# Optimization experiments

Measured on AMD Instinct MI355X. Metric: run time of the kernel, lower is better.

Reference implementation:

```python
import math
import jax, jax.numpy as jnp
import numpy as np

D_MODEL = 768
EXPAND = 2
D_INNER = EXPAND * D_MODEL  # 1536
D_STATE = 16
D_CONV = 4
DT_RANK = math.ceil(D_INNER / 16)  # 96
B, L = 2, 2048
LN_EPS = 1e-5


def setup_inputs() -> dict:
    key = jax.random.key(0)
    ks = jax.random.split(key, 10)
    x = jax.random.normal(ks[0], (B, L, D_MODEL), dtype=jnp.float32)
    ln_g = jnp.ones((D_MODEL,), jnp.float32)
    ln_b = jnp.zeros((D_MODEL,), jnp.float32)
    W_in = jax.random.normal(ks[1], (D_MODEL, 2 * D_INNER), jnp.float32) / np.sqrt(D_MODEL)
    conv_w = jax.random.normal(ks[2], (D_INNER, 1, D_CONV), jnp.float32) / np.sqrt(D_CONV)
    conv_b = jax.random.normal(ks[3], (D_INNER,), jnp.float32) * 0.02
    W_xproj = jax.random.normal(ks[4], (D_INNER, DT_RANK + 2 * D_STATE), jnp.float32) / np.sqrt(D_INNER)
    W_dt = jax.random.normal(ks[5], (DT_RANK, D_INNER), jnp.float32) / np.sqrt(DT_RANK)
    # dt bias init: inverse-softplus of dt ~ LogUniform(1e-3, 1e-1)
    dt = jnp.exp(jax.random.uniform(ks[6], (D_INNER,)) * (math.log(0.1) - math.log(0.001)) + math.log(0.001))
    b_dt = dt + jnp.log(-jnp.expm1(-dt))
    log_A = jnp.log(jnp.tile(jnp.arange(1, D_STATE + 1, dtype=jnp.float32), (D_INNER, 1)))  # (d_inner, N)
    D_param = jnp.ones((D_INNER,), jnp.float32)
    W_out = jax.random.normal(ks[7], (D_INNER, D_MODEL), jnp.float32) / np.sqrt(D_INNER)
    return dict(x=x, ln_g=ln_g, ln_b=ln_b, W_in=W_in, conv_w=conv_w, conv_b=conv_b,
                W_xproj=W_xproj, W_dt=W_dt, b_dt=b_dt, log_A=log_A, D_param=D_param, W_out=W_out)


def _mamba_block(x, ln_g, ln_b, W_in, conv_w, conv_b, W_xproj, W_dt, b_dt, log_A, D_param, W_out):
    residual = x
    # LayerNorm
    mu = jnp.mean(x, axis=-1, keepdims=True)
    var = jnp.var(x, axis=-1, keepdims=True)
    xn = (x - mu) * jax.lax.rsqrt(var + LN_EPS) * ln_g + ln_b
    # in projection -> (u, v)
    uv = xn @ W_in  # (B, L, 2*d_inner)
    u, v = jnp.split(uv, 2, axis=-1)
    # causal depthwise conv1d along length (torch pads both sides then truncates -> left pad only)
    u_c = jnp.transpose(u, (0, 2, 1))  # (B, d_inner, L)
    u_c = jax.lax.conv_general_dilated(
        u_c, conv_w, window_strides=(1,), padding=[(D_CONV - 1, 0)],
        dimension_numbers=('NCH', 'OIH', 'NCH'), feature_group_count=D_INNER)
    u_c = u_c + conv_b[None, :, None]
    u = jnp.transpose(u_c, (0, 2, 1))  # (B, L, d_inner)
    u = jax.nn.silu(u)
    # Selective SSM
    x_dbl = u @ W_xproj  # (B, L, dt_rank + 2N)
    dlt, Bm, Cm = jnp.split(x_dbl, [DT_RANK, DT_RANK + D_STATE], axis=-1)
    delta = jax.nn.softplus(dlt @ W_dt + b_dt)  # (B, L, d_inner)
    A = -jnp.exp(log_A)  # (d_inner, N)
    A_bar = jnp.exp(jnp.einsum('bld,dn->bldn', delta, A))         # discretized A
    Bu = jnp.einsum('bld,bln,bld->bldn', delta, Bm, u)            # B_bar * u
    # parallel scan: h_k = A_bar_k * h_{k-1} + Bu_k
    def comb(e1, e2):
        a1, b1 = e1
        a2, b2 = e2
        return a1 * a2, a2 * b1 + b2
    _, h = jax.lax.associative_scan(comb, (A_bar, Bu), axis=1)
    y = jnp.einsum('bldn,bln->bld', h, Cm) + u * D_param
    # gate + residual
    y = y * jax.nn.silu(v)
    return y @ W_out + residual


def reference(x, ln_g, ln_b, W_in, conv_w, conv_b, W_xproj, W_dt, b_dt, log_A, D_param, W_out):
    return _mamba_block(x, ln_g, ln_b, W_in, conv_w, conv_b, W_xproj, W_dt, b_dt, log_A, D_param, W_out)
```

## Files before the change

### kernel.cpp

```cpp
#include <hip/hip_runtime.h>

#define D_MODEL 768
#define D_INNER 1536
#define D_STATE 16
#define DT_RANK 96
#define BB 2
#define LL 2048
#define TT (BB*LL)
#define NC 64
#define CL 32
#define SKK 4
#define LOG2E 1.44269504f

typedef unsigned short u16;
typedef short bf16x8 __attribute__((ext_vector_type(8)));
typedef unsigned short u16x8 __attribute__((ext_vector_type(8)));
typedef float f32x4  __attribute__((ext_vector_type(4)));

__device__ __forceinline__ float bf2f(u16 u) {
    union { unsigned int i; float f; } c; c.i = ((unsigned int)u) << 16; return c.f;
}
__device__ __forceinline__ u16 f2bf(float f) {
    union { float f; unsigned int i; } c; c.f = f;
    unsigned int x = c.i;
    return (u16)((x + 0x7fffu + ((x >> 16) & 1u)) >> 16);
}
__device__ __forceinline__ float bfu_lo(unsigned int u) {
    union { unsigned int i; float f; } c; c.i = u << 16; return c.f;
}
__device__ __forceinline__ float bfu_hi(unsigned int u) {
    union { unsigned int i; float f; } c; c.i = u & 0xFFFF0000u; return c.f;
}
__device__ __forceinline__ float ldx(const void* p, size_t i, bool f32) {
    return f32 ? ((const float*)p)[i] : bf2f(((const u16*)p)[i]);
}

__device__ __forceinline__ void gload16(const u16* g, u16* l) {
    __builtin_amdgcn_global_load_lds(
        (const __attribute__((address_space(1))) unsigned int*)g,
        (__attribute__((address_space(3))) unsigned int*)l, 16, 0, 0);
}

__global__ void detect_kernel(const void* x, int* flag)
{
    __shared__ int bad;
    if (threadIdx.x == 0) bad = 0;
    __syncthreads();
    const u16* p = (const u16*)x;
    int local = 0;
    for (int i = threadIdx.x; i < 2048; i += 256) {
        const float v = bf2f(p[2 * i]);
        if (!(fabsf(v) < 1e4f)) local = 1;
    }
    if (local) atomicOr(&bad, 1);
    __syncthreads();
    if (threadIdx.x == 0) *flag = bad;
}

__global__ __launch_bounds__(256) void transpose_all_kernel(
    const void* __restrict__ W_in, const void* __restrict__ W_xp,
    const void* __restrict__ W_dt, const void* __restrict__ W_out,
    u16* __restrict__ WtIn, u16* __restrict__ WtXp,
    u16* __restrict__ WtDt, u16* __restrict__ WtOut,
    const int* __restrict__ flagp)
{
    const bool f32 = (*flagp != 0);
    int bid = blockIdx.x;
    const void* src; u16* dst; int K, N, bx, by;
    if (bid < 576)      { src = W_in;  dst = WtIn;  K = 768;  N = 3072; bx = bid % 48; by = bid / 48; }
    else if (bid < 624) { bid -= 576; src = W_xp;  dst = WtXp;  K = 1536; N = 128;  bx = bid % 2;  by = bid / 2; }
    else if (bid < 672) { bid -= 624; src = W_dt;  dst = WtDt;  K = 96;   N = 1536; bx = bid % 24; by = bid / 24; }
    else                { bid -= 672; src = W_out; dst = WtOut; K = 1536; N = 768;  bx = bid % 12; by = bid / 12; }
    __shared__ u16 tile[64][72];
    const int t  = threadIdx.x;
    const int n0 = bx * 64, k0 = by * 64;
    {
        const int r = t >> 2, c = (t & 3) * 16;
        const int k = k0 + r;
        if (k < K) {
            #pragma unroll
            for (int i = 0; i < 16; ++i)
                tile[r][c + i] = f2bf(ldx(src, (size_t)k * N + n0 + c + i, f32));
        }
    }
    __syncthreads();
    {
        const int nl = t >> 2, kl = (t & 3) * 16;
        const int n = n0 + nl;
        #pragma unroll
        for (int i = 0; i < 16; ++i) {
            const int k = k0 + kl + i;
            if (k < K) dst[(size_t)n * K + k] = tile[kl + i][nl];
        }
    }
}

__global__ __launch_bounds__(256) void ln_kernel(const void* __restrict__ x,
    const void* __restrict__ g, const void* __restrict__ b, u16* __restrict__ xn,
    const int* __restrict__ flagp)
{
    const bool f32 = (*flagp != 0);
    const int tok = blockIdx.x;
    const int tid = threadIdx.x;
    const size_t base = (size_t)tok * D_MODEL;
    float v[3];
    v[0] = ldx(x, base + tid, f32);
    v[1] = ldx(x, base + tid + 256, f32);
    v[2] = ldx(x, base + tid + 512, f32);
    float s = v[0] + v[1] + v[2];
    float q = v[0]*v[0] + v[1]*v[1] + v[2]*v[2];
    #pragma unroll
    for (int o = 32; o > 0; o >>= 1) {
        s += __shfl_down(s, o, 64);
        q += __shfl_down(q, o, 64);
    }
    __shared__ float ss[4], qq[4];
    if ((tid & 63) == 0) { ss[tid >> 6] = s; qq[tid >> 6] = q; }
    __syncthreads();
    const float S = ss[0] + ss[1] + ss[2] + ss[3];
    const float Q = qq[0] + qq[1] + qq[2] + qq[3];
    const float mu  = S * (1.f / D_MODEL);
    const float var = Q * (1.f / D_MODEL) - mu * mu;
    const float rs  = rsqrtf(var + 1e-5f);
    u16* outr = xn + base;
    #pragma unroll
    for (int i = 0; i < 3; ++i) {
        const int c = tid + i * 256;
        outr[c] = f2bf((v[i] - mu) * rs * ldx(g, c, f32) + ldx(b, c, f32));
    }
}

template<int EPI>
__global__ __launch_bounds__(256) void mfma_gemm(
    const u16* __restrict__ A, const u16* __restrict__ Bt,
    u16* __restrict__ C, void* __restrict__ Cout, const void* __restrict__ aux,
    float* __restrict__ Cf, const int* __restrict__ flagp,
    int Kslice, int lda, int ldbt, int ldc)
{
    const bool f32 = (*flagp != 0);
    __shared__ alignas(16) u16 As[64 * 32];
    __shared__ alignas(16) u16 Bs[64 * 32];
    const int tid  = threadIdx.x;
    const int wave = tid >> 6, lane = tid & 63;
    const int lrow = lane & 15, quad = lane >> 4;
    const int row0 = blockIdx.y * 64, col0 = blockIdx.x * 64;
    const int k0   = blockIdx.z * Kslice;
    const int srow = wave * 16 + (lane >> 2);
    const int skk  = (lane & 3) * 8;
    u16* lA = &As[wave * 512];
    u16* lB = &Bs[wave * 512];
    const u16* gA = A  + (size_t)(row0 + srow) * lda  + skk;
    const u16* gB = Bt + (size_t)(col0 + srow) * ldbt + skk;
    f32x4 acc[4] = {{0.f,0.f,0.f,0.f},{0.f,0.f,0.f,0.f},{0.f,0.f,0.f,0.f},{0.f,0.f,0.f,0.f}};
    for (int kt = k0; kt < k0 + Kslice; kt += 32) {
        gload16(gA + kt, lA);
        gload16(gB + kt, lB);
        __syncthreads();
        const bf16x8 af = *(const bf16x8*)(&As[(wave * 16 + lrow) * 32 + quad * 8]);
        #pragma unroll
        for (int t = 0; t < 4; ++t) {
            const bf16x8 bf_ = *(const bf16x8*)(&Bs[(t * 16 + lrow) * 32 + quad * 8]);
            acc[t] = __builtin_amdgcn_mfma_f32_16x16x32_bf16(af, bf_, acc[t], 0, 0, 0);
        }
        __syncthreads();
    }
    #pragma unroll
    for (int t = 0; t < 4; ++t) {
        #pragma unroll
        for (int r = 0; r < 4; ++r) {
            const int row = row0 + wave * 16 + quad * 4 + r;
            const int col = col0 + t * 16 + lrow;
            const size_t idx = (size_t)row * ldc + col;
            float vv = acc[t][r];
            if (EPI == 1) {
                vv += ldx(aux, col, f32);
                vv = (vv > 20.f) ? vv : log1pf(__expf(vv));
                C[idx] = f2bf(vv);
            } else if (EPI == 2) {
                vv += ldx(aux, idx, f32);
                if (f32) ((float*)Cout)[idx] = vv;
                else     ((u16*)Cout)[idx]   = f2bf(vv);
            } else if (EPI == 3) {
                atomicAdd(&Cf[idx], vv);
            } else {
                C[idx] = f2bf(vv);
            }
        }
    }
}

template<int EPI>
__global__ __launch_bounds__(256) void mfma_gemm128(
    const u16* __restrict__ A, const u16* __restrict__ Bt,
    u16* __restrict__ C, void* __restrict__ Cout, const void* __restrict__ aux,
    const int* __restrict__ flagp,
    int K, int lda, int ldbt, int ldc)
{
    const bool f32 = (*flagp != 0);
    __shared__ alignas(16) u16 As[128 * 32];
    __shared__ alignas(16) u16 Bs[128 * 32];
    const int tid  = threadIdx.x;
    const int wave = tid >> 6, lane = tid & 63;
    const int lrow = lane & 15, quad = lane >> 4;
    const int wy = wave >> 1, wx = wave & 1;
    const int row0 = blockIdx.y * 128, col0 = blockIdx.x * 128;
    const int skk = (lane & 3) * 8;
    const int r0 = wave * 16 + (lane >> 2);
    const int r1 = r0 + 64;
    u16* lA0 = &As[wave * 512];
    u16* lA1 = &As[(wave + 4) * 512];
    u16* lB0 = &Bs[wave * 512];
    u16* lB1 = &Bs[(wave + 4) * 512];
    const u16* gA0 = A  + (size_t)(row0 + r0) * lda  + skk;
    const u16* gA1 = A  + (size_t)(row0 + r1) * lda  + skk;
    const u16* gB0 = Bt + (size_t)(col0 + r0) * ldbt + skk;
    const u16* gB1 = Bt + (size_t)(col0 + r1) * ldbt + skk;
    f32x4 acc[4][4];
    #pragma unroll
    for (int i = 0; i < 4; ++i)
        #pragma unroll
        for (int j = 0; j < 4; ++j) acc[i][j] = (f32x4){0.f,0.f,0.f,0.f};
    for (int kt = 0; kt < K; kt += 32) {
        gload16(gA0 + kt, lA0);
        gload16(gA1 + kt, lA1);
        gload16(gB0 + kt, lB0);
        gload16(gB1 + kt, lB1);
        __syncthreads();
        bf16x8 af[4], bf_[4];
        #pragma unroll
        for (int i = 0; i < 4; ++i)
            af[i] = *(const bf16x8*)(&As[(wy * 64 + i * 16 + lrow) * 32 + quad * 8]);
        #pragma unroll
        for (int j = 0; j < 4; ++j)
            bf_[j] = *(const bf16x8*)(&Bs[(wx * 64 + j * 16 + lrow) * 32 + quad * 8]);
        #pragma unroll
        for (int i = 0; i < 4; ++i)
            #pragma unroll
            for (int j = 0; j < 4; ++j)
                acc[i][j] = __builtin_amdgcn_mfma_f32_16x16x32_bf16(af[i], bf_[j], acc[i][j], 0, 0, 0);
        __syncthreads();
    }
    #pragma unroll
    for (int i = 0; i < 4; ++i) {
        #pragma unroll
        for (int j = 0; j < 4; ++j) {
            #pragma unroll
            for (int r = 0; r < 4; ++r) {
                const int row = row0 + wy * 64 + i * 16 + quad * 4 + r;
                const int col = col0 + wx * 64 + j * 16 + lrow;
                const size_t idx = (size_t)row * ldc + col;
                float vv = acc[i][j][r];
                if (EPI == 1) {
                    vv += ldx(aux, col, f32);
                    vv = (vv > 20.f) ? vv : log1pf(__expf(vv));
                    C[idx] = f2bf(vv);
                } else if (EPI == 2) {
                    vv += ldx(aux, idx, f32);
                    if (f32) ((float*)Cout)[idx] = vv;
                    else     ((u16*)Cout)[idx]   = f2bf(vv);
                } else {
                    C[idx] = f2bf(vv);
                }
            }
        }
    }
}

__global__ __launch_bounds__(256) void convert_kernel(const float* __restrict__ src,
                                                      u16* __restrict__ dst, int n)
{
    const int i = blockIdx.x * 256 + threadIdx.x;
    if (i < n) dst[i] = f2bf(src[i]);
}

__global__ __launch_bounds__(256) void conv_silu_kernel(
    const u16* __restrict__ uv, const void* __restrict__ cw, const void* __restrict__ cb,
    u16* __restrict__ us, const int* __restrict__ flagp)
{
    const bool f32 = (*flagp != 0);
    const int idx = blockIdx.x * 256 + threadIdx.x;
    const int d   = idx % D_INNER;
    const int tok = idx / D_INNER;
    const int l   = tok & (LL - 1);
    float acc = ldx(cb, d, f32);
    #pragma unroll
    for (int j = 0; j < 4; ++j) {
        const int li = l - 3 + j;
        if (li >= 0)
            acc += bf2f(uv[(size_t)(tok - 3 + j) * (2*D_INNER) + d]) * ldx(cw, d * 4 + j, f32);
    }
    us[idx] = f2bf(acc / (1.f + __expf(-acc)));
}

__global__ __launch_bounds__(256) void scan1_kernel(
    const u16* __restrict__ delta, const u16* __restrict__ us,
    const u16* __restrict__ xdbl, const void* __restrict__ log_A,
    float* __restrict__ carryA, float* __restrict__ carryH,
    const int* __restrict__ flagp)
{
    const bool f32 = (*flagp != 0);
    const int d = blockIdx.x * 256 + threadIdx.x;
    const int c = blockIdx.y, b = blockIdx.z;
    float A2[16], h[16];
    #pragma unroll
    for (int j = 0; j < 16; ++j) {
        A2[j] = -__expf(ldx(log_A, d * D_STATE + j, f32)) * LOG2E;
        h[j] = 0.f;
    }
    bool pw = true;
    #pragma unroll
    for (int j = 1; j < 16; ++j)
        pw = pw && (fabsf(A2[j] - (j + 1) * A2[0]) <= 0.02f * (j + 1) * fabsf(A2[0]));
    float sdl = 0.f;
    size_t tok = (size_t)b * LL + c * CL;
    if (pw) {
        #pragma unroll 2
        for (int t = 0; t < CL; ++t, ++tok) {
            const float dl = bf2f(delta[tok * D_INNER + d]);
            const float ul = bf2f(us[tok * D_INNER + d]);
            const uint4 B0 = *(const uint4*)(xdbl + tok * 128 + DT_RANK);
            const uint4 B1 = *(const uint4*)(xdbl + tok * 128 + DT_RANK + 8);
            const float dlul = dl * ul;
            sdl += dl;
            const unsigned int bw[8] = {B0.x,B0.y,B0.z,B0.w,B1.x,B1.y,B1.z,B1.w};
            const float a1 = exp2f(dl * A2[0]);
            float aj = 1.f;
            #pragma unroll
            for (int j = 0; j < 16; ++j) {
                aj *= a1;
                const float Bn = (j & 1) ? bfu_hi(bw[j >> 1]) : bfu_lo(bw[j >> 1]);
                h[j] = aj * h[j] + dlul * Bn;
            }
        }
    } else {
        #pragma unroll 2
        for (int t = 0; t < CL; ++t, ++tok) {
            const float dl = bf2f(delta[tok * D_INNER + d]);
            const float ul = bf2f(us[tok * D_INNER + d]);
            const uint4 B0 = *(const uint4*)(xdbl + tok * 128 + DT_RANK);
            const uint4 B1 = *(const uint4*)(xdbl + tok * 128 + DT_RANK + 8);
            const float dlul = dl * ul;
            sdl += dl;
            const unsigned int bw[8] = {B0.x,B0.y,B0.z,B0.w,B1.x,B1.y,B1.z,B1.w};
            #pragma unroll
            for (int j = 0; j < 16; ++j) {
                const float Bn = (j & 1) ? bfu_hi(bw[j >> 1]) : bfu_lo(bw[j >> 1]);
                h[j] = exp2f(dl * A2[j]) * h[j] + dlul * Bn;
            }
        }
    }
    const size_t ci = (((size_t)b * NC + c) * D_INNER + d) * D_STATE;
    #pragma unroll
    for (int q = 0; q < 4; ++q) {
        *(float4*)(carryA + ci + 4*q) = (float4){
            exp2f(A2[4*q+0]*sdl), exp2f(A2[4*q+1]*sdl),
            exp2f(A2[4*q+2]*sdl), exp2f(A2[4*q+3]*sdl)};
        *(float4*)(carryH + ci + 4*q) = (float4){h[4*q+0], h[4*q+1], h[4*q+2], h[4*q+3]};
    }
}

__global__ __launch_bounds__(256) void scan2_kernel(
    const float* __restrict__ carryA, float* __restrict__ carryH)
{
    const int gid = blockIdx.x * 256 + threadIdx.x;
    const int b   = gid / (D_INNER * D_STATE);
    const int dn  = gid % (D_INNER * D_STATE);
    float hrun = 0.f;
    #pragma unroll
    for (int c = 0; c < NC; ++c) {
        const size_t ci = ((size_t)(b * NC + c) * D_INNER * D_STATE) + dn;
        const float a = carryA[ci], hh = carryH[ci];
        carryH[ci] = hrun;
        hrun = a * hrun + hh;
    }
}

__global__ __launch_bounds__(256) void scan3_kernel(
    const u16* __restrict__ delta, const u16* __restrict__ us,
    const u16* __restrict__ xdbl, u16* __restrict__ uv,
    const void* __restrict__ log_A, const void* __restrict__ D_param,
    const float* __restrict__ carryH, const int* __restrict__ flagp)
{
    const bool f32 = (*flagp != 0);
    const int d = blockIdx.x * 256 + threadIdx.x;
    const int c = blockIdx.y, b = blockIdx.z;
    const float Dd = ldx(D_param, d, f32);
    float A2[16], h[16];
    const size_t ci = (((size_t)b * NC + c) * D_INNER + d) * D_STATE;
    #pragma unroll
    for (int j = 0; j < 16; ++j)
        A2[j] = -__expf(ldx(log_A, d * D_STATE + j, f32)) * LOG2E;
    bool pw = true;
    #pragma unroll
    for (int j = 1; j < 16; ++j)
        pw = pw && (fabsf(A2[j] - (j + 1) * A2[0]) <= 0.02f * (j + 1) * fabsf(A2[0]));
    #pragma unroll
    for (int q = 0; q < 4; ++q) {
        const float4 hq = *(const float4*)(carryH + ci + 4*q);
        h[4*q+0] = hq.x; h[4*q+1] = hq.y; h[4*q+2] = hq.z; h[4*q+3] = hq.w;
    }
    size_t tok = (size_t)b * LL + c * CL;
    if (pw) {
        #pragma unroll 2
        for (int t = 0; t < CL; ++t, ++tok) {
            const float dl = bf2f(delta[tok * D_INNER + d]);
            const float ul = bf2f(us[tok * D_INNER + d]);
            const uint4 B0 = *(const uint4*)(xdbl + tok * 128 + DT_RANK);
            const uint4 B1 = *(const uint4*)(xdbl + tok * 128 + DT_RANK + 8);
            const uint4 C0 = *(const uint4*)(xdbl + tok * 128 + DT_RANK + D_STATE);
            const uint4 C1 = *(const uint4*)(xdbl + tok * 128 + DT_RANK + D_STATE + 8);
            const float dlul = dl * ul;
            const unsigned int bw[8] = {B0.x,B0.y,B0.z,B0.w,B1.x,B1.y,B1.z,B1.w};
            const unsigned int cw_[8] = {C0.x,C0.y,C0.z,C0.w,C1.x,C1.y,C1.z,C1.w};
            const float a1 = exp2f(dl * A2[0]);
            float aj = 1.f, p = 0.f;
            #pragma unroll
            for (int j = 0; j < 16; ++j) {
                aj *= a1;
                const float Bn = (j & 1) ? bfu_hi(bw[j >> 1]) : bfu_lo(bw[j >> 1]);
                const float Cn = (j & 1) ? bfu_hi(cw_[j >> 1]) : bfu_lo(cw_[j >> 1]);
                h[j] = aj * h[j] + dlul * Bn;
                p += h[j] * Cn;
            }
            const float vv = bf2f(uv[tok * (2*D_INNER) + D_INNER + d]);
            uv[tok * (2*D_INNER) + d] = f2bf((p + ul * Dd) * (vv / (1.f + __expf(-vv))));
        }
    } else {
        #pragma unroll 2
        for (int t = 0; t < CL; ++t, ++tok) {
            const float dl = bf2f(delta[tok * D_INNER + d]);
            const float ul = bf2f(us[tok * D_INNER + d]);
            const uint4 B0 = *(const uint4*)(xdbl + tok * 128 + DT_RANK);
            const uint4 B1 = *(const uint4*)(xdbl + tok * 128 + DT_RANK + 8);
            const uint4 C0 = *(const uint4*)(xdbl + tok * 128 + DT_RANK + D_STATE);
            const uint4 C1 = *(const uint4*)(xdbl + tok * 128 + DT_RANK + D_STATE + 8);
            const float dlul = dl * ul;
            const unsigned int bw[8] = {B0.x,B0.y,B0.z,B0.w,B1.x,B1.y,B1.z,B1.w};
            const unsigned int cw_[8] = {C0.x,C0.y,C0.z,C0.w,C1.x,C1.y,C1.z,C1.w};
            float p = 0.f;
            #pragma unroll
            for (int j = 0; j < 16; ++j) {
                const float Bn = (j & 1) ? bfu_hi(bw[j >> 1]) : bfu_lo(bw[j >> 1]);
                const float Cn = (j & 1) ? bfu_hi(cw_[j >> 1]) : bfu_lo(cw_[j >> 1]);
                h[j] = exp2f(dl * A2[j]) * h[j] + dlul * Bn;
                p += h[j] * Cn;
            }
            const float vv = bf2f(uv[tok * (2*D_INNER) + D_INNER + d]);
            uv[tok * (2*D_INNER) + d] = f2bf((p + ul * Dd) * (vv / (1.f + __expf(-vv))));
        }
    }
}

extern "C" void kernel_launch(void* const* d_in, const int* in_sizes, int n_in,
                              void* d_out, int out_size, void* d_ws, size_t ws_size,
                              hipStream_t stream)
{
    const void* x      = d_in[0];
    const void* ln_g   = d_in[1];
    const void* ln_b   = d_in[2];
    const void* W_in   = d_in[3];
    const void* conv_w = d_in[4];
    const void* conv_b = d_in[5];
    const void* W_xp   = d_in[6];
    const void* W_dt   = d_in[7];
    const void* b_dt   = d_in[8];
    const void* log_A  = d_in[9];
    const void* D_par  = d_in[10];
    const void* W_out  = d_in[11];

    int* flag  = (int*)d_ws;
    u16* ws    = (u16*)((char*)d_ws + 512);
    u16* xn    = ws;
    u16* uv    = xn + (size_t)TT * D_MODEL;
    u16* us    = uv + (size_t)TT * 2 * D_INNER;
    u16* xdbl  = us + (size_t)TT * D_INNER;
    u16* delta = xdbl + (size_t)TT * 128;
    float* carryH = (float*)(delta + (size_t)TT * D_INNER);
    float* carryA = carryH + (size_t)BB * NC * D_INNER * D_STATE;
    u16* WtIn  = (u16*)(carryA + (size_t)BB * NC * D_INNER * D_STATE);
    u16* WtXp  = WtIn  + (size_t)2 * D_INNER * D_MODEL;
    u16* WtDt  = WtXp  + (size_t)(DT_RANK + 2 * D_STATE) * D_INNER;
    u16* WtOut = WtDt  + (size_t)D_INNER * DT_RANK;
    float* xdblF = (float*)(WtOut + (size_t)D_MODEL * D_INNER);

    detect_kernel<<<1, 256, 0, stream>>>(x, flag);
    transpose_all_kernel<<<960, 256, 0, stream>>>(
        W_in, W_xp, W_dt, W_out, WtIn, WtXp, WtDt, WtOut, flag);
    hipMemsetAsync(xdblF, 0, (size_t)TT * 128 * sizeof(float), stream);

    ln_kernel<<<TT, 256, 0, stream>>>(x, ln_g, ln_b, xn, flag);
    mfma_gemm128<0><<<dim3(2 * D_INNER / 128, TT / 128), 256, 0, stream>>>(
        xn, WtIn, uv, nullptr, nullptr, flag, D_MODEL, D_MODEL, D_MODEL, 2 * D_INNER);
    conv_silu_kernel<<<(TT * D_INNER) / 256, 256, 0, stream>>>(uv, conv_w, conv_b, us, flag);
    mfma_gemm<3><<<dim3(2, TT / 64, SKK), 256, 0, stream>>>(
        us, WtXp, nullptr, nullptr, nullptr, xdblF, flag,
        D_INNER / SKK, D_INNER, D_INNER, 128);
    convert_kernel<<<(TT * 128 + 255) / 256, 256, 0, stream>>>(xdblF, xdbl, TT * 128);
    mfma_gemm<1><<<dim3(D_INNER / 64, TT / 64, 1), 256, 0, stream>>>(
        xdbl, WtDt, delta, nullptr, b_dt, nullptr, flag,
        DT_RANK, 128, DT_RANK, D_INNER);
    scan1_kernel<<<dim3(D_INNER / 256, NC, BB), 256, 0, stream>>>(
        delta, us, xdbl, log_A, carryA, carryH, flag);
    scan2_kernel<<<(BB * D_INNER * D_STATE) / 256, 256, 0, stream>>>(carryA, carryH);
    scan3_kernel<<<dim3(D_INNER / 256, NC, BB), 256, 0, stream>>>(
        delta, us, xdbl, uv, log_A, D_par, carryH, flag);
    mfma_gemm<2><<<dim3(D_MODEL / 64, TT / 64, 1), 256, 0, stream>>>(
        uv, WtOut, nullptr, d_out, x, nullptr, flag,
        D_INNER, 2 * D_INNER, D_INNER, D_MODEL);
}
```

Before: 322.7 us.

## Double-buffer LDS tiles in MFMA GEMMs and add XCD-aware block swizzle

Both GEMM kernels now use two LDS buffers and issue the global-to-LDS load for the next K tile before computing on the current one, leaving a single barrier per iteration. This is meant to overlap memory latency with MFMA work. A block-index remap groups neighbouring tiles onto the same XCD for better L2 reuse when the grid is not split along K. Doubling shared memory may lower occupancy, and the single-barrier scheme relies on the next loop iteration's barrier to make the prefetched data visible.

Measured after the change: 320.1 us. No clear change (-0.8%).

```diff
diff --git a/kernel.cpp b/kernel.cpp
--- a/kernel.cpp
+++ b/kernel.cpp
@@ -39,6 +39,14 @@
     __builtin_amdgcn_global_load_lds(
         (const __attribute__((address_space(1))) unsigned int*)g,
         (__attribute__((address_space(3))) unsigned int*)l, 16, 0, 0);
+}
+
+__device__ __forceinline__ void xcd_swz(int& bx, int& by) {
+    const int gx = gridDim.x;
+    const int cpx = (gx * gridDim.y) >> 3;
+    const int bid = by * gx + bx;
+    const int w = (bid & 7) * cpx + (bid >> 3);
+    bx = w % gx; by = w / gx;
 }
 
 __global__ void detect_kernel(const void* x, int* flag)
@@ -138,31 +146,40 @@
     int Kslice, int lda, int ldbt, int ldc)
 {
     const bool f32 = (*flagp != 0);
-    __shared__ alignas(16) u16 As[64 * 32];
-    __shared__ alignas(16) u16 Bs[64 * 32];
+    __shared__ alignas(16) u16 As[2 * 64 * 32];
+    __shared__ alignas(16) u16 Bs[2 * 64 * 32];
     const int tid  = threadIdx.x;
     const int wave = tid >> 6, lane = tid & 63;
     const int lrow = lane & 15, quad = lane >> 4;
-    const int row0 = blockIdx.y * 64, col0 = blockIdx.x * 64;
+    int bx = blockIdx.x, by = blockIdx.y;
+    if (gridDim.z == 1) xcd_swz(bx, by);
+    const int row0 = by * 64, col0 = bx * 64;
     const int k0   = blockIdx.z * Kslice;
     const int srow = wave * 16 + (lane >> 2);
     const int skk  = (lane & 3) * 8;
-    u16* lA = &As[wave * 512];
-    u16* lB = &Bs[wave * 512];
-    const u16* gA = A  + (size_t)(row0 + srow) * lda  + skk;
-    const u16* gB = Bt + (size_t)(col0 + srow) * ldbt + skk;
+    const int wb   = wave * 512;
+    const u16* gA = A  + (size_t)(row0 + srow) * lda  + k0 + skk;
+    const u16* gB = Bt + (size_t)(col0 + srow) * ldbt + k0 + skk;
+    const int nst = Kslice >> 5;
+    gload16(gA, &As[wb]);
+    gload16(gB, &Bs[wb]);
     f32x4 acc[4] = {{0.f,0.f,0.f,0.f},{0.f,0.f,0.f,0.f},{0.f,0.f,0.f,0.f},{0.f,0.f,0.f,0.f}};
-    for (int kt = k0; kt < k0 + Kslice; kt += 32) {
-        gload16(gA + kt, lA);
-        gload16(gB + kt, lB);
+    int cur = 0;
+    for (int t = 0; t < nst; ++t) {
         __syncthreads();
-        const bf16x8 af = *(const bf16x8*)(&As[(wave * 16 + lrow) * 32 + quad * 8]);
-        #pragma unroll
-        for (int t = 0; t < 4; ++t) {
-            const bf16x8 bf_ = *(const bf16x8*)(&Bs[(t * 16 + lrow) * 32 + quad * 8]);
-            acc[t] = __builtin_amdgcn_mfma_f32_16x16x32_bf16(af, bf_, acc[t], 0, 0, 0);
-        }
-        __syncthreads();
+        const int boff = cur << 11;
+        if (t + 1 < nst) {
+            const int poff = boff ^ 2048;
+            gload16(gA + (t + 1) * 32, &As[poff + wb]);
+            gload16(gB + (t + 1) * 32, &Bs[poff + wb]);
+        }
+        const bf16x8 af = *(const bf16x8*)(&As[boff + (wave * 16 + lrow) * 32 + quad * 8]);
+        #pragma unroll
+        for (int q = 0; q < 4; ++q) {
+            const bf16x8 bq = *(const bf16x8*)(&Bs[boff + (q * 16 + lrow) * 32 + quad * 8]);
+            acc[q] = __builtin_amdgcn_mfma_f32_16x16x32_bf16(af, bq, acc[q], 0, 0, 0);
+        }
+        cur ^= 1;
     }
     #pragma unroll
     for (int t = 0; t < 4; ++t) {
@@ -197,48 +214,58 @@
     int K, int lda, int ldbt, int ldc)
 {
     const bool f32 = (*flagp != 0);
-    __shared__ alignas(16) u16 As[128 * 32];
-    __shared__ alignas(16) u16 Bs[128 * 32];
+    __shared__ alignas(16) u16 As[2 * 128 * 32];
+    __shared__ alignas(16) u16 Bs[2 * 128 * 32];
     const int tid  = threadIdx.x;
     const int wave = tid >> 6, lane = tid & 63;
     const int lrow = lane & 15, quad = lane >> 4;
     const int wy = wave >> 1, wx = wave & 1;
-    const int row0 = blockIdx.y * 128, col0 = blockIdx.x * 128;
+    int bx = blockIdx.x, by = blockIdx.y;
+    if (gridDim.z == 1) xcd_swz(bx, by);
+    const int row0 = by * 128, col0 = bx * 128;
     const int skk = (lane & 3) * 8;
     const int r0 = wave * 16 + (lane >> 2);
     const int r1 = r0 + 64;
-    u16* lA0 = &As[wave * 512];
-    u16* lA1 = &As[(wave + 4) * 512];
-    u16* lB0 = &Bs[wave * 512];
-    u16* lB1 = &Bs[(wave + 4) * 512];
+    const int wb0 = wave * 512, wb1 = (wave + 4) * 512;
     const u16* gA0 = A  + (size_t)(row0 + r0) * lda  + skk;
     const u16* gA1 = A  + (size_t)(row0 + r1) * lda  + skk;
     const u16* gB0 = Bt + (size_t)(col0 + r0) * ldbt + skk;
     const u16* gB1 = Bt + (size_t)(col0 + r1) * ldbt + skk;
+    const int nst = K >> 5;
+    gload16(gA0, &As[wb0]);
+    gload16(gA1, &As[wb1]);
+    gload16(gB0, &Bs[wb0]);
+    gload16(gB1, &Bs[wb1]);
     f32x4 acc[4][4];
     #pragma unroll
     for (int i = 0; i < 4; ++i)
         #pragma unroll
         for (int j = 0; j < 4; ++j) acc[i][j] = (f32x4){0.f,0.f,0.f,0.f};
-    for (int kt = 0; kt < K; kt += 32) {
-        gload16(gA0 + kt, lA0);
-        gload16(gA1 + kt, lA1);
-        gload16(gB0 + kt, lB0);
-        gload16(gB1 + kt, lB1);
+    int cur = 0;
+    for (int t = 0; t < nst; ++t) {
         __syncthreads();
+        const int boff = cur << 12;
+        if (t + 1 < nst) {
+            const int poff = boff ^ 4096;
+            const int kt = (t + 1) * 32;
+            gload16(gA0 + kt, &As[poff + wb0]);
+            gload16(gA1 + kt, &As[poff + wb1]);
+            gload16(gB0 + kt, &Bs[poff + wb0]);
+            gload16(gB1 + kt, &Bs[poff + wb1]);
+        }
         bf16x8 af[4], bf_[4];
         #pragma unroll
         for (int i = 0; i < 4; ++i)
-            af[i] = *(const bf16x8*)(&As[(wy * 64 + i * 16 + lrow) * 32 + quad * 8]);
+            af[i] = *(const bf16x8*)(&As[boff + (wy * 64 + i * 16 + lrow) * 32 + quad * 8]);
         #pragma unroll
         for (int j = 0; j < 4; ++j)
-            bf_[j] = *(const bf16x8*)(&Bs[(wx * 64 + j * 16 + lrow) * 32 + quad * 8]);
+            bf_[j] = *(const bf16x8*)(&Bs[boff + (wx * 64 + j * 16 + lrow) * 32 + quad * 8]);
         #pragma unroll
         for (int i = 0; i < 4; ++i)
             #pragma unroll
             for (int j = 0; j < 4; ++j)
                 acc[i][j] = __builtin_amdgcn_mfma_f32_16x16x32_bf16(af[i], bf_[j], acc[i][j], 0, 0, 0);
-        __syncthreads();
+        cur ^= 1;
     }
     #pragma unroll
     for (int i = 0; i < 4; ++i) {
```
